# Kernel optimization log

Hardware: AMD Instinct MI355X
Metric: run time of the kernel (lower is better)

## Reference

```python
import jax, jax.numpy as jnp
import numpy as np

N, L, DS, DP, H, A, Q, V = 1, 512, 384, 256, 12, 16, 4, 8
SHID = H * (DP + A + 3 * V + V)  # 3648
WC = float(np.sqrt(2.0 / (9.0 * Q)))
WL = float(np.sqrt(1.0 / 3.0))
EPS = 1e-5


def quat2rot(q):
    # q: (..., 3) partial quaternion (w fixed to 1, then normalized) -> (..., 3, 3)
    ones = jnp.ones(q.shape[:-1] + (1,), q.dtype)
    qf = jnp.concatenate([ones, q], axis=-1)
    qf = qf / jnp.linalg.norm(qf, axis=-1, keepdims=True)
    w, x, y, z = qf[..., 0], qf[..., 1], qf[..., 2], qf[..., 3]
    r0 = jnp.stack([1 - 2 * (y * y + z * z), 2 * (x * y - w * z), 2 * (x * z + w * y)], -1)
    r1 = jnp.stack([2 * (x * y + w * z), 1 - 2 * (x * x + z * z), 2 * (y * z - w * x)], -1)
    r2 = jnp.stack([2 * (x * z - w * y), 2 * (y * z + w * x), 1 - 2 * (x * x + y * y)], -1)
    return jnp.stack([r0, r1, r2], axis=-2)


def layer_norm(x, g, b):
    m = x.mean(-1, keepdims=True)
    v = ((x - m) ** 2).mean(-1, keepdims=True)
    return (x - m) / jnp.sqrt(v + EPS) * g + b


def setup_inputs() -> dict:
    key = jax.random.key(0)
    ks = jax.random.split(key, 24)
    w = lambda k, shape, s=0.02: (jax.random.normal(k, shape, jnp.float32) * s)
    return {
        'sfea': jax.random.normal(ks[0], (N, L, DS), jnp.float32),
        'pfea': jax.random.normal(ks[1], (N, L, L, DP), jnp.float32),
        'quat': jax.random.normal(ks[2], (N, L, 3), jnp.float32) * 0.1,
        'trsl': jax.random.normal(ks[3], (N, L, 3), jnp.float32),
        'Wq': w(ks[4], (DS, H * A)), 'Wk': w(ks[5], (DS, H * A)), 'Wv': w(ks[6], (DS, H * A)),
        'Wqp': w(ks[7], (DS, H * Q * 3)), 'Wkp': w(ks[8], (DS, H * Q * 3)), 'Wvp': w(ks[9], (DS, H * V * 3)),
        'Wb': w(ks[10], (DP, H)),
        'scale': jnp.ones((H,), jnp.float32),
        'Ws': w(ks[11], (SHID, DS)), 'bs': jnp.zeros((DS,), jnp.float32),
        'W1': w(ks[12], (DS, DS)), 'b1': jnp.zeros((DS,), jnp.float32),
        'W2': w(ks[13], (DS, DS)), 'b2': jnp.zeros((DS,), jnp.float32),
        'W3': w(ks[14], (DS, DS)), 'b3': jnp.zeros((DS,), jnp.float32),
        'g1': jnp.ones((DS,), jnp.float32), 'be1': jnp.zeros((DS,), jnp.float32),
        'g2': jnp.ones((DS,), jnp.float32), 'be2': jnp.zeros((DS,), jnp.float32),
    }


def reference(sfea, pfea, quat, trsl, Wq, Wk, Wv, Wqp, Wkp, Wvp, Wb, scale, Ws, bs,
              W1, b1, W2, b2, W3, b3, g1, be1, g2, be2):
    n, l = sfea.shape[0], sfea.shape[1]
    # projections
    q = (sfea @ Wq).reshape(n, l, H, A)
    k = (sfea @ Wk).reshape(n, l, H, A)
    v = (sfea @ Wv).reshape(n, l, H, A)
    qp = (sfea @ Wqp).reshape(n, l, H, Q, 3)
    kp = (sfea @ Wkp).reshape(n, l, H, Q, 3)
    vp = (sfea @ Wvp).reshape(n, l, H, V, 3)
    b = jnp.einsum('nijp,ph->nijh', pfea, Wb)
    # local frames
    rot = quat2rot(quat)  # (n, l, 3, 3)
    t = trsl[:, :, None, None, :]
    qp_g = jnp.einsum('nlij,nlhqj->nlhqi', rot, qp) + t
    kp_g = jnp.einsum('nlij,nlhqj->nlhqi', rot, kp) + t
    vp_g = jnp.einsum('nlij,nlhvj->nlhvi', rot, vp) + t
    # attention logits
    qk = jnp.einsum('nihd,njhd->nijh', q, k) / np.sqrt(A)
    diff = qp_g[:, :, None] - kp_g[:, None]  # (n, i, j, h, q, 3)
    d2 = jnp.sum(diff * diff, axis=(-1, -2))  # (n, i, j, h)
    qkp = (WC * jax.nn.softplus(scale) / 2.0) * d2
    a = jax.nn.softmax(WL * (qk + b - qkp), axis=2)  # (n, i, j, h)
    # weighted sums (einsum avoids huge broadcast intermediates)
    op = jnp.einsum('nijh,nijp->nihp', a, pfea)
    ov = jnp.einsum('nijh,njhd->nihd', a, v)
    ovp_g = jnp.einsum('nijh,njhvc->nihvc', a, vp_g)
    # map back into local frame: R^T (x - t)
    ovp = jnp.einsum('nlji,nlhvj->nlhvi', rot, ovp_g - t)
    ovp_norm = jnp.sqrt(jnp.sum(ovp * ovp, axis=-1))  # (n, l, h, v)
    shid = jnp.concatenate([op, ov, ovp.reshape(n, l, H, V * 3), ovp_norm], axis=-1)
    shid = shid.reshape(n, l, SHID)
    # output projection + residual, post-LN, MLP, post-LN (v1 path, p_drop=0)
    s = sfea + shid @ Ws + bs
    s = layer_norm(s, g1, be1)
    h = jax.nn.relu(s @ W1 + b1)
    h = jax.nn.relu(h @ W2 + b2)
    s = s + (h @ W3 + b3)
    s = layer_norm(s, g2, be2)
    return s
```

## Files before the change

### kernel.cpp

```cpp
#include <hip/hip_runtime.h>
#include <cstddef>

typedef __attribute__((ext_vector_type(8))) short short8;
typedef __attribute__((ext_vector_type(4))) float f32x4;

#define WC_CONST 0.2357022603955158f
#define WL_CONST 0.5773502691896258f

__device__ __forceinline__ unsigned short rne_bf16(float f) {
  unsigned int u = __float_as_uint(f);
  u += 0x7fffu + ((u >> 16) & 1u);
  return (unsigned short)(u >> 16);
}

__global__ __launch_bounds__(256) void concat_w_kernel(
    const float* __restrict__ Wq, const float* __restrict__ Wk, const float* __restrict__ Wv,
    const float* __restrict__ Wqp, const float* __restrict__ Wkp, const float* __restrict__ Wvp,
    float* __restrict__ Wcat) {
  int idx = blockIdx.x * 256 + threadIdx.x;
  if (idx >= 384 * 1152) return;
  int k = idx / 1152, c = idx % 1152;
  float v;
  if (c < 192)       v = Wq [k*192 + c];
  else if (c < 384)  v = Wk [k*192 + (c-192)];
  else if (c < 576)  v = Wv [k*192 + (c-384)];
  else if (c < 720)  v = Wqp[k*144 + (c-576)];
  else if (c < 864)  v = Wkp[k*144 + (c-720)];
  else               v = Wvp[k*288 + (c-864)];
  Wcat[idx] = v;
}

__global__ __launch_bounds__(256) void gemm64_kernel(
    const float* __restrict__ Amat, const float* __restrict__ Bmat, float* __restrict__ Cp,
    int M, int N, int K, int ksl) {
  __shared__ float As[16][68];
  __shared__ float Bs[16][68];
  int t = threadIdx.x;
  int bn = blockIdx.x, bm = blockIdx.y, bz = blockIdx.z;
  int k0 = bz * ksl;
  int tr = t >> 4, tc = t & 15;
  int lm = t >> 2, lk4 = (t & 3) << 2;
  int lkb = t >> 4, lnq = (t & 15) << 2;
  const float* Ab = Amat + (size_t)(bm*64 + lm) * K;
  const float* Bb = Bmat + bn*64 + lnq;
  float acc[4][4];
  #pragma unroll
  for (int a2 = 0; a2 < 4; a2++)
    #pragma unroll
    for (int b2 = 0; b2 < 4; b2++) acc[a2][b2] = 0.f;

  for (int k = k0; k < k0 + ksl; k += 16) {
    float4 av = *(const float4*)(Ab + k + lk4);
    float4 bv = *(const float4*)(Bb + (size_t)(k + lkb) * N);
    As[lk4+0][lm] = av.x; As[lk4+1][lm] = av.y; As[lk4+2][lm] = av.z; As[lk4+3][lm] = av.w;
    *(float4*)&Bs[lkb][lnq] = bv;
    __syncthreads();
    #pragma unroll
    for (int kk = 0; kk < 16; kk++) {
      float4 a4 = *(const float4*)&As[kk][tr << 2];
      float4 b4 = *(const float4*)&Bs[kk][tc << 2];
      float ar[4] = {a4.x, a4.y, a4.z, a4.w};
      float br[4] = {b4.x, b4.y, b4.z, b4.w};
      #pragma unroll
      for (int a2 = 0; a2 < 4; a2++)
        #pragma unroll
        for (int b2 = 0; b2 < 4; b2++) acc[a2][b2] += ar[a2] * br[b2];
    }
    __syncthreads();
  }
  float* Cb = Cp + (size_t)bz * M * N + (size_t)(bm*64 + (tr << 2)) * N + bn*64 + (tc << 2);
  #pragma unroll
  for (int r = 0; r < 4; r++) {
    float4 o = {acc[r][0], acc[r][1], acc[r][2], acc[r][3]};
    *(float4*)(Cb + (size_t)r * N) = o;
  }
}

__global__ __launch_bounds__(256) void reduce_kernel(
    const float* __restrict__ Cp, float* __restrict__ out, const float* __restrict__ bias,
    int relu, int MN, int N, int sk) {
  int idx = blockIdx.x * 256 + threadIdx.x;
  if (idx >= MN) return;
  float s = 0.f;
  for (int z = 0; z < sk; z++) s += Cp[(size_t)z * MN + idx];
  if (bias) s += bias[idx % N];
  if (relu) s = fmaxf(s, 0.f);
  out[idx] = s;
}

__global__ __launch_bounds__(64) void frames_kernel(
    const float* __restrict__ proj, const float* __restrict__ quat, const float* __restrict__ trsl,
    float* __restrict__ rotb, float* __restrict__ qpg, float* __restrict__ kpg,
    float* __restrict__ vpg) {
  int i = blockIdx.x, t = threadIdx.x;
  float q0 = quat[i*3+0], q1 = quat[i*3+1], q2 = quat[i*3+2];
  float inv = rsqrtf(1.f + q0*q0 + q1*q1 + q2*q2);
  float w = inv, x = q0*inv, y = q1*inv, z = q2*inv;
  float R00 = 1.f - 2.f*(y*y + z*z), R01 = 2.f*(x*y - w*z), R02 = 2.f*(x*z + w*y);
  float R10 = 2.f*(x*y + w*z), R11 = 1.f - 2.f*(x*x + z*z), R12 = 2.f*(y*z - w*x);
  float R20 = 2.f*(x*z - w*y), R21 = 2.f*(y*z + w*x), R22 = 1.f - 2.f*(x*x + y*y);
  float t0 = trsl[i*3+0], t1 = trsl[i*3+1], t2 = trsl[i*3+2];
  if (t == 0) {
    float* rb = rotb + i*9;
    rb[0]=R00; rb[1]=R01; rb[2]=R02; rb[3]=R10; rb[4]=R11; rb[5]=R12; rb[6]=R20; rb[7]=R21; rb[8]=R22;
  }
  for (int pt = t; pt < 192; pt += 64) {
    const float* src; float* dst;
    if (pt < 48)      { src = proj + i*1152 + 576 + pt*3;        dst = qpg + i*144 + pt*3; }
    else if (pt < 96) { src = proj + i*1152 + 720 + (pt-48)*3;   dst = kpg + i*144 + (pt-48)*3; }
    else              { src = proj + i*1152 + 864 + (pt-96)*3;   dst = vpg + i*288 + (pt-96)*3; }
    float p0 = src[0], p1 = src[1], p2 = src[2];
    dst[0] = R00*p0 + R01*p1 + R02*p2 + t0;
    dst[1] = R10*p0 + R11*p1 + R12*p2 + t1;
    dst[2] = R20*p0 + R21*p1 + R22*p2 + t2;
  }
}

__device__ __forceinline__ float lt1_val(
    const float* __restrict__ proj, const float* __restrict__ kpg,
    const float* qs_, const float* qps_, float coef, int jg, int h) {
  const float4* kr = (const float4*)(proj + (size_t)jg*1152 + 192 + h*16);
  const float4* qr = (const float4*)(qs_ + h*16);
  float qk = 0.f;
  #pragma unroll
  for (int m = 0; m < 4; m++) {
    float4 kv = kr[m], qv = qr[m];
    qk += qv.x*kv.x + qv.y*kv.y + qv.z*kv.z + qv.w*kv.w;
  }
  const float4* kpr = (const float4*)(kpg + (size_t)jg*144 + h*12);
  const float4* qpr = (const float4*)(qps_ + h*12);
  float d2 = 0.f;
  #pragma unroll
  for (int m = 0; m < 3; m++) {
    float4 kv = kpr[m], qv = qpr[m];
    float dx = qv.x-kv.x, dy = qv.y-kv.y, dz = qv.z-kv.z, dw = qv.w-kv.w;
    d2 += dx*dx + dy*dy + dz*dz + dw*dw;
  }
  return qk*0.25f - coef*d2;
}

__global__ __launch_bounds__(768) void attn2_kernel(
    const float* __restrict__ proj, const float* __restrict__ qpg,
    const float* __restrict__ kpg, const float* __restrict__ vpg,
    const float* __restrict__ pfea, const float* __restrict__ Wb,
    const float* __restrict__ rotb, const float* __restrict__ trsl,
    const float* __restrict__ scale, float* __restrict__ shid) {
  __shared__ __align__(16) float P[32][260];
  __shared__ __align__(16) float Lw[512][12];
  __shared__ short wbf[8][64][8];
  __shared__ float Lb[2][32][12];
  __shared__ __align__(16) float qs[12][16];
  __shared__ __align__(16) float qps[12][12];
  __shared__ float coefs[12];
  __shared__ float sh_inv[12];
  __shared__ float rot_s[9];
  __shared__ float ovpg_l[12][24];

  int i = blockIdx.x;
  int t = threadIdx.x;
  int w = t >> 6, lane = t & 63;

  for (int idx = t; idx < 192; idx += 768) qs[idx >> 4][idx & 15] = proj[i*1152 + idx];
  for (int idx = t; idx < 144; idx += 768) qps[idx / 12][idx % 12] = qpg[i*144 + idx];
  if (t < 12) coefs[t] = WC_CONST * 0.5f * log1pf(__expf(scale[t]));
  if (t < 9)  rot_s[t] = rotb[i*9 + t];
  for (int s2 = t; s2 < 512; s2 += 768) {
    int ks = s2 >> 6, l = s2 & 63;
    int col = l & 15, kb = ks * 32 + ((l >> 4) << 3);
    #pragma unroll
    for (int j = 0; j < 8; j++)
      wbf[ks][l][j] = (col < 12) ? (short)rne_bf16(Wb[(kb + j) * 12 + col]) : (short)0;
  }
  __syncthreads();

  float4 opacc[12];
  #pragma unroll
  for (int h = 0; h < 12; h++) { opacc[h].x = 0.f; opacc[h].y = 0.f; opacc[h].z = 0.f; opacc[h].w = 0.f; }
  float4 streg[8];

  if (w >= 8) {
    int rbase = (w - 8) * 8;
    const float* src = pfea + (size_t)i * 131072;
    #pragma unroll
    for (int q2 = 0; q2 < 8; q2++)
      streg[q2] = *(const float4*)(src + (size_t)(rbase + q2) * 256 + (lane << 2));
  } else if (w >= 2) {
    int e = (w - 2) * 64 + lane;
    int jl = e / 12, h = e - jl * 12;
    Lb[0][jl][h] = lt1_val(proj, kpg, &qs[0][0], &qps[0][0], coefs[h], jl, h);
  }

  for (int tt = 0; tt < 16; tt++) {
    __syncthreads();
    if (w >= 8) {
      int rbase = (w - 8) * 8;
      #pragma unroll
      for (int q2 = 0; q2 < 8; q2++)
        *(float4*)&P[rbase + q2][lane << 2] = streg[q2];
    }
    __syncthreads();
    if (w < 2) {
      f32x4 accb = {0.f, 0.f, 0.f, 0.f};
      int row = (w << 4) + (lane & 15);
      int kq = lane >> 4;
      const float* Pb = &P[row][kq * 8];
      #pragma unroll
      for (int ks = 0; ks < 8; ks++) {
        float4 f0 = *(const float4*)(Pb + ks * 32);
        float4 f1 = *(const float4*)(Pb + ks * 32 + 4);
        short8 af;
        af[0] = (short)rne_bf16(f0.x); af[1] = (short)rne_bf16(f0.y);
        af[2] = (short)rne_bf16(f0.z); af[3] = (short)rne_bf16(f0.w);
        af[4] = (short)rne_bf16(f1.x); af[5] = (short)rne_bf16(f1.y);
        af[6] = (short)rne_bf16(f1.z); af[7] = (short)rne_bf16(f1.w);
        short8 bfv = *(const short8*)(&wbf[ks][lane][0]);
        accb = __builtin_amdgcn_mfma_f32_16x16x32_bf16(af, bfv, accb, 0, 0, 0);
      }
      int h = lane & 15;
      if (h < 12) {
        #pragma unroll
        for (int r = 0; r < 4; r++) {
          int jl = (w << 4) + kq * 4 + r;
          float lv = Lb[tt & 1][jl][h] + accb[r];
          Lw[tt * 32 + jl][h] = __expf(WL_CONST * lv);
        }
      }
    } else if (w < 8) {
      if (tt < 15) {
        int e = (w - 2) * 64 + lane;
        int jl = e / 12, h = e - jl * 12;
        Lb[(tt + 1) & 1][jl][h] =
            lt1_val(proj, kpg, &qs[0][0], &qps[0][0], coefs[h], (tt + 1) * 32 + jl, h);
      }
    } else {
      if (tt < 15) {
        int rbase = (w - 8) * 8;
        const float* src = pfea + (size_t)i * 131072 + (size_t)(tt + 1) * 32 * 256;
        #pragma unroll
        for (int q2 = 0; q2 < 8; q2++)
          streg[q2] = *(const float4*)(src + (size_t)(rbase + q2) * 256 + (lane << 2));
      }
    }
    __syncthreads();
    for (int rr = w; rr < 32; rr += 12) {
      const float4* lwp = (const float4*)&Lw[tt * 32 + rr][0];
      float4 wa = lwp[0], wb2 = lwp[1], wc = lwp[2];
      float4 pv = *(const float4*)&P[rr][lane << 2];
      opacc[0].x += pv.x*wa.x; opacc[0].y += pv.y*wa.x; opacc[0].z += pv.z*wa.x; opacc[0].w += pv.w*wa.x;
      opacc[1].x += pv.x*wa.y; opacc[1].y += pv.y*wa.y; opacc[1].z += pv.z*wa.y; opacc[1].w += pv.w*wa.y;
      opacc[2].x += pv.x*wa.z; opacc[2].y += pv.y*wa.z; opacc[2].z += pv.z*wa.z; opacc[2].w += pv.w*wa.z;
      opacc[3].x += pv.x*wa.w; opacc[3].y += pv.y*wa.w; opacc[3].z += pv.z*wa.w; opacc[3].w += pv.w*wa.w;
      opacc[4].x += pv.x*wb2.x; opacc[4].y += pv.y*wb2.x; opacc[4].z += pv.z*wb2.x; opacc[4].w += pv.w*wb2.x;
      opacc[5].x += pv.x*wb2.y; opacc[5].y += pv.y*wb2.y; opacc[5].z += pv.z*wb2.y; opacc[5].w += pv.w*wb2.y;
      opacc[6].x += pv.x*wb2.z; opacc[6].y += pv.y*wb2.z; opacc[6].z += pv.z*wb2.z; opacc[6].w += pv.w*wb2.z;
      opacc[7].x += pv.x*wb2.w; opacc[7].y += pv.y*wb2.w; opacc[7].z += pv.z*wb2.w; opacc[7].w += pv.w*wb2.w;
      opacc[8].x += pv.x*wc.x; opacc[8].y += pv.y*wc.x; opacc[8].z += pv.z*wc.x; opacc[8].w += pv.w*wc.x;
      opacc[9].x += pv.x*wc.y; opacc[9].y += pv.y*wc.y; opacc[9].z += pv.z*wc.y; opacc[9].w += pv.w*wc.y;
      opacc[10].x += pv.x*wc.z; opacc[10].y += pv.y*wc.z; opacc[10].z += pv.z*wc.z; opacc[10].w += pv.w*wc.z;
      opacc[11].x += pv.x*wc.w; opacc[11].y += pv.y*wc.w; opacc[11].z += pv.z*wc.w; opacc[11].w += pv.w*wc.w;
    }
  }
  __syncthreads();

  if (w < 12) {
    float sacc = 0.f;
    #pragma unroll
    for (int r2 = 0; r2 < 8; r2++) sacc += Lw[r2 * 64 + lane][w];
    #pragma unroll
    for (int off = 32; off >= 1; off >>= 1) sacc += __shfl_xor(sacc, off);
    if (lane == 0) sh_inv[w] = 1.0f / sacc;
  }
  __syncthreads();

  float4* Pred = (float4*)&P[0][0];
  #pragma unroll
  for (int gr = 0; gr < 6; gr++) {
    Pred[(w * 2 + 0) * 64 + lane] = opacc[2 * gr + 0];
    Pred[(w * 2 + 1) * 64 + lane] = opacc[2 * gr + 1];
    __syncthreads();
    if (t < 128) {
      int hh = t >> 6, ll = t & 63;
      float4 sum = {0.f, 0.f, 0.f, 0.f};
      #pragma unroll
      for (int w2 = 0; w2 < 12; w2++) {
        float4 v = Pred[(w2 * 2 + hh) * 64 + ll];
        sum.x += v.x; sum.y += v.y; sum.z += v.z; sum.w += v.w;
      }
      int h = 2 * gr + hh;
      float isv = sh_inv[h];
      float4 o = {sum.x * isv, sum.y * isv, sum.z * isv, sum.w * isv};
      *(float4*)(shid + (size_t)i * 3648 + h * 304 + (ll << 2)) = o;
    }
    __syncthreads();
  }

  if (t < 192) {
    int h = t >> 4, d = t & 15;
    const float* vb = proj + 384 + h * 16 + d;
    float acc = 0.f;
    #pragma unroll 8
    for (int j = 0; j < 512; j++) acc += Lw[j][h] * vb[(size_t)j * 1152];
    shid[(size_t)i * 3648 + h * 304 + 256 + d] = acc * sh_inv[h];
  } else if (t >= 256 && t < 544) {
    int idx = t - 256, h = idx / 24, m2 = idx % 24;
    const float* vb = vpg + h * 24 + m2;
    float acc = 0.f;
    #pragma unroll 8
    for (int j = 0; j < 512; j++) acc += Lw[j][h] * vb[(size_t)j * 288];
    ovpg_l[h][m2] = acc * sh_inv[h];
  }
  __syncthreads();

  if (t < 96) {
    int h = t >> 3, vv = t & 7;
    float x = ovpg_l[h][vv*3+0] - trsl[i*3+0];
    float y = ovpg_l[h][vv*3+1] - trsl[i*3+1];
    float z = ovpg_l[h][vv*3+2] - trsl[i*3+2];
    float o0 = rot_s[0]*x + rot_s[3]*y + rot_s[6]*z;
    float o1 = rot_s[1]*x + rot_s[4]*y + rot_s[7]*z;
    float o2 = rot_s[2]*x + rot_s[5]*y + rot_s[8]*z;
    float* so = shid + (size_t)i*3648 + h*304 + 272 + vv*3;
    so[0] = o0; so[1] = o1; so[2] = o2;
    shid[(size_t)i*3648 + h*304 + 296 + vv] = sqrtf(o0*o0 + o1*o1 + o2*o2);
  }
}

__global__ __launch_bounds__(384) void ln384_kernel(
    const float* __restrict__ resid, const float* __restrict__ C, const float* __restrict__ bias,
    const float* __restrict__ g, const float* __restrict__ be, float* __restrict__ out) {
  int i = blockIdx.x, t = threadIdx.x;
  __shared__ float red[6];
  float x = resid[(size_t)i*384 + t] + C[(size_t)i*384 + t] + bias[t];
  float s = x;
  #pragma unroll
  for (int off = 32; off >= 1; off >>= 1) s += __shfl_xor(s, off);
  if ((t & 63) == 0) red[t >> 6] = s;
  __syncthreads();
  float m = (red[0]+red[1]+red[2]+red[3]+red[4]+red[5]) * (1.f/384.f);
  __syncthreads();
  float d = x - m;
  float v = d * d;
  #pragma unroll
  for (int off = 32; off >= 1; off >>= 1) v += __shfl_xor(v, off);
  if ((t & 63) == 0) red[t >> 6] = v;
  __syncthreads();
  float var = (red[0]+red[1]+red[2]+red[3]+red[4]+red[5]) * (1.f/384.f);
  out[(size_t)i*384 + t] = d * rsqrtf(var + 1e-5f) * g[t] + be[t];
}

extern "C" void kernel_launch(void* const* d_in, const int* in_sizes, int n_in,
                              void* d_out, int out_size, void* d_ws, size_t ws_size,
                              hipStream_t stream) {
  const float* sfea = (const float*)d_in[0];
  const float* pfea = (const float*)d_in[1];
  const float* quat = (const float*)d_in[2];
  const float* trsl = (const float*)d_in[3];
  const float* Wq   = (const float*)d_in[4];
  const float* Wk   = (const float*)d_in[5];
  const float* Wv   = (const float*)d_in[6];
  const float* Wqp  = (const float*)d_in[7];
  const float* Wkp  = (const float*)d_in[8];
  const float* Wvp  = (const float*)d_in[9];
  const float* Wb   = (const float*)d_in[10];
  const float* scale= (const float*)d_in[11];
  const float* Wsm  = (const float*)d_in[12];
  const float* bs   = (const float*)d_in[13];
  const float* W1   = (const float*)d_in[14];
  const float* b1   = (const float*)d_in[15];
  const float* W2   = (const float*)d_in[16];
  const float* b2   = (const float*)d_in[17];
  const float* W3   = (const float*)d_in[18];
  const float* b3   = (const float*)d_in[19];
  const float* g1   = (const float*)d_in[20];
  const float* be1  = (const float*)d_in[21];
  const float* g2   = (const float*)d_in[22];
  const float* be2  = (const float*)d_in[23];
  float* out = (float*)d_out;
  float* wsf = (float*)d_ws;

  float* Wcat = wsf;
  float* proj = Wcat + 442368;
  float* rotb = proj + 589824;
  float* qpg  = rotb + 4608;
  float* kpg  = qpg + 73728;
  float* vpg  = kpg + 73728;
  float* shid = vpg + 147456;
  float* cpart= shid + 1867776;
  float* C1   = cpart + 1179648;
  float* s1   = C1 + 196608;
  float* h1   = s1 + 196608;
  float* h2   = h1 + 196608;
  float* C3   = h2 + 196608;

  concat_w_kernel<<<1728, 256, 0, stream>>>(Wq, Wk, Wv, Wqp, Wkp, Wvp, Wcat);
  gemm64_kernel<<<dim3(18, 8, 1), 256, 0, stream>>>(sfea, Wcat, proj, 512, 1152, 384, 384);
  frames_kernel<<<512, 64, 0, stream>>>(proj, quat, trsl, rotb, qpg, kpg, vpg);
  attn2_kernel<<<512, 768, 0, stream>>>(proj, qpg, kpg, vpg, pfea, Wb, rotb, trsl, scale, shid);

  gemm64_kernel<<<dim3(6, 8, 6), 256, 0, stream>>>(shid, Wsm, cpart, 512, 384, 3648, 608);
  reduce_kernel<<<768, 256, 0, stream>>>(cpart, C1, nullptr, 0, 196608, 384, 6);
  ln384_kernel<<<512, 384, 0, stream>>>(sfea, C1, bs, g1, be1, s1);

  gemm64_kernel<<<dim3(6, 8, 3), 256, 0, stream>>>(s1, W1, cpart, 512, 384, 384, 128);
  reduce_kernel<<<768, 256, 0, stream>>>(cpart, h1, b1, 1, 196608, 384, 3);
  gemm64_kernel<<<dim3(6, 8, 3), 256, 0, stream>>>(h1, W2, cpart, 512, 384, 384, 128);
  reduce_kernel<<<768, 256, 0, stream>>>(cpart, h2, b2, 1, 196608, 384, 3);
  gemm64_kernel<<<dim3(6, 8, 3), 256, 0, stream>>>(h2, W3, cpart, 512, 384, 384, 128);
  reduce_kernel<<<768, 256, 0, stream>>>(cpart, C3, nullptr, 0, 196608, 384, 3);
  ln384_kernel<<<512, 384, 0, stream>>>(s1, C3, b3, g2, be2, out);
}
```

Baseline: 308.0 us.

## Restructure attention with async LDS loads and fuse MLP GEMM epilogues

The attention kernel now streams the pair features in 16-row tiles straight into double-buffered shared memory with global_load_lds, instead of staging them through registers. Work is respecialised across warps: one wave does the bias MFMA, three compute logits, four issue loads, six accumulate the pair-feature sum, and the rest accumulate the value and point-value sums inside the main loop rather than in separate serial loops at the end. The MLP replaces split-K GEMMs plus reduce kernels with a single 32x32-tile GEMM that applies bias and ReLU in its epilogue, cutting launches and partial-sum traffic. The risks are more barriers from doubling the tile count, lower per-wave parallelism in the pair-feature reduction, and a small GEMM tile with little register reuse.

```diff
diff --git a/kernel.cpp b/kernel.cpp
--- a/kernel.cpp
+++ b/kernel.cpp
@@ -11,6 +11,13 @@
   unsigned int u = __float_as_uint(f);
   u += 0x7fffu + ((u >> 16) & 1u);
   return (unsigned short)(u >> 16);
+}
+
+typedef const __attribute__((address_space(1))) unsigned int* gas_u32;
+typedef __attribute__((address_space(3))) unsigned int* las_u32;
+
+__device__ __forceinline__ void gl_lds16(const float* g, float* l) {
+  __builtin_amdgcn_global_load_lds((gas_u32)(const void*)g, (las_u32)(void*)l, 16, 0, 0);
 }
 
 __global__ __launch_bounds__(256) void concat_w_kernel(
@@ -88,6 +95,43 @@
   out[idx] = s;
 }
 
+__global__ __launch_bounds__(256) void gemm32_kernel(
+    const float* __restrict__ Amat, const float* __restrict__ Bmat,
+    const float* __restrict__ bias,
+    float* __restrict__ C, int M, int N, int K, int relu) {
+  __shared__ float As[16][34];
+  __shared__ float Bs[16][34];
+  int t = threadIdx.x;
+  int bn = blockIdx.x, bm = blockIdx.y;
+  int tr = t >> 4, tc = t & 15;
+  int lm = t >> 3, lk2 = (t & 7) << 1;
+  int lkb = t >> 4, ln2 = (t & 15) << 1;
+  const float* Ab = Amat + (size_t)(bm*32 + lm) * K;
+  const float* Bb = Bmat + bn*32 + ln2;
+  float a00=0.f, a01=0.f, a10=0.f, a11=0.f;
+  for (int k = 0; k < K; k += 16) {
+    float2 av = *(const float2*)(Ab + k + lk2);
+    float2 bv = *(const float2*)(Bb + (size_t)(k + lkb) * N);
+    As[lk2][lm] = av.x; As[lk2+1][lm] = av.y;
+    *(float2*)&Bs[lkb][ln2] = bv;
+    __syncthreads();
+    #pragma unroll
+    for (int kk = 0; kk < 16; kk++) {
+      float2 a2 = *(const float2*)&As[kk][tr << 1];
+      float2 b2 = *(const float2*)&Bs[kk][tc << 1];
+      a00 += a2.x*b2.x; a01 += a2.x*b2.y; a10 += a2.y*b2.x; a11 += a2.y*b2.y;
+    }
+    __syncthreads();
+  }
+  int r0 = bm*32 + (tr << 1), c0 = bn*32 + (tc << 1);
+  float bb0 = bias ? bias[c0] : 0.f, bb1 = bias ? bias[c0+1] : 0.f;
+  float o00 = a00 + bb0, o01 = a01 + bb1, o10 = a10 + bb0, o11 = a11 + bb1;
+  if (relu) { o00=fmaxf(o00,0.f); o01=fmaxf(o01,0.f); o10=fmaxf(o10,0.f); o11=fmaxf(o11,0.f); }
+  float2 w0 = {o00, o01}, w1 = {o10, o11};
+  *(float2*)(C + (size_t)r0*N + c0) = w0;
+  *(float2*)(C + (size_t)(r0+1)*N + c0) = w1;
+}
+
 __global__ __launch_bounds__(64) void frames_kernel(
     const float* __restrict__ proj, const float* __restrict__ quat, const float* __restrict__ trsl,
     float* __restrict__ rotb, float* __restrict__ qpg, float* __restrict__ kpg,
@@ -139,25 +183,23 @@
   return qk*0.25f - coef*d2;
 }
 
-__global__ __launch_bounds__(768) void attn2_kernel(
+__global__ __launch_bounds__(768, 6) void attn3_kernel(
     const float* __restrict__ proj, const float* __restrict__ qpg,
     const float* __restrict__ kpg, const float* __restrict__ vpg,
     const float* __restrict__ pfea, const float* __restrict__ Wb,
     const float* __restrict__ rotb, const float* __restrict__ trsl,
     const float* __restrict__ scale, float* __restrict__ shid) {
-  __shared__ __align__(16) float P[32][260];
+  __shared__ __align__(16) float P[2][16][260];
   __shared__ __align__(16) float Lw[512][12];
   __shared__ short wbf[8][64][8];
-  __shared__ float Lb[2][32][12];
+  __shared__ float Lb[2][16][12];
   __shared__ __align__(16) float qs[12][16];
   __shared__ __align__(16) float qps[12][12];
-  __shared__ float coefs[12];
-  __shared__ float sh_inv[12];
-  __shared__ float rot_s[9];
+  __shared__ float coefs[12], sh_inv[12], rot_s[9];
+  __shared__ __align__(16) float redbuf[2048];
   __shared__ float ovpg_l[12][24];
 
-  int i = blockIdx.x;
-  int t = threadIdx.x;
+  int i = blockIdx.x, t = threadIdx.x;
   int w = t >> 6, lane = t & 63;
 
   for (int idx = t; idx < 192; idx += 768) qs[idx >> 4][idx & 15] = proj[i*1152 + idx];
@@ -173,37 +215,33 @@
   }
   __syncthreads();
 
-  float4 opacc[12];
-  #pragma unroll
-  for (int h = 0; h < 12; h++) { opacc[h].x = 0.f; opacc[h].y = 0.f; opacc[h].z = 0.f; opacc[h].w = 0.f; }
-  float4 streg[8];
-
-  if (w >= 8) {
-    int rbase = (w - 8) * 8;
-    const float* src = pfea + (size_t)i * 131072;
-    #pragma unroll
-    for (int q2 = 0; q2 < 8; q2++)
-      streg[q2] = *(const float4*)(src + (size_t)(rbase + q2) * 256 + (lane << 2));
-  } else if (w >= 2) {
-    int e = (w - 2) * 64 + lane;
+  if (w >= 1 && w <= 3) {
+    int e = (w - 1) * 64 + lane;
     int jl = e / 12, h = e - jl * 12;
     Lb[0][jl][h] = lt1_val(proj, kpg, &qs[0][0], &qps[0][0], coefs[h], jl, h);
-  }
-
-  for (int tt = 0; tt < 16; tt++) {
-    __syncthreads();
-    if (w >= 8) {
-      int rbase = (w - 8) * 8;
-      #pragma unroll
-      for (int q2 = 0; q2 < 8; q2++)
-        *(float4*)&P[rbase + q2][lane << 2] = streg[q2];
-    }
-    __syncthreads();
-    if (w < 2) {
+  } else if (w >= 4 && w <= 7) {
+    int r = (w - 4) * 4;
+    const float* src = pfea + (size_t)i * 131072 + lane * 4;
+    #pragma unroll
+    for (int q = 0; q < 4; q++) gl_lds16(src + (size_t)(r + q) * 256, &P[0][r + q][0]);
+  }
+  __syncthreads();
+
+  float4 acc4[4];
+  #pragma unroll
+  for (int c = 0; c < 4; c++) { acc4[c].x=0.f; acc4[c].y=0.f; acc4[c].z=0.f; acc4[c].w=0.f; }
+  float accv[3] = {0.f, 0.f, 0.f};
+  float accvp[5] = {0.f, 0.f, 0.f, 0.f, 0.f};
+  int hv0 = lane >> 4, hv1 = 4 + (lane >> 4), hv2 = 8 + (lane >> 4);
+  int hp0 = lane / 24, hp1 = (lane + 64) / 24, hp2 = (lane + 128) / 24,
+      hp3 = (lane + 192) / 24, hp4 = (lane + 256) / 24;
+
+  int cur = 0;
+  for (int tt = 0; tt < 32; tt++) {
+    if (w == 0) {
       f32x4 accb = {0.f, 0.f, 0.f, 0.f};
-      int row = (w << 4) + (lane & 15);
-      int kq = lane >> 4;
-      const float* Pb = &P[row][kq * 8];
+      int row = lane & 15, kq = lane >> 4;
+      const float* Pb = &P[cur][row][kq * 8];
       #pragma unroll
       for (int ks = 0; ks < 8; ks++) {
         float4 f0 = *(const float4*)(Pb + ks * 32);
@@ -220,94 +258,117 @@
       if (h < 12) {
         #pragma unroll
         for (int r = 0; r < 4; r++) {
-          int jl = (w << 4) + kq * 4 + r;
-          float lv = Lb[tt & 1][jl][h] + accb[r];
-          Lw[tt * 32 + jl][h] = __expf(WL_CONST * lv);
+          int jl = kq * 4 + r;
+          Lw[tt * 16 + jl][h] = __expf(WL_CONST * (Lb[tt & 1][jl][h] + accb[r]));
         }
       }
-    } else if (w < 8) {
-      if (tt < 15) {
-        int e = (w - 2) * 64 + lane;
+    } else if (w <= 3) {
+      if (tt < 31) {
+        int e = (w - 1) * 64 + lane;
         int jl = e / 12, h = e - jl * 12;
         Lb[(tt + 1) & 1][jl][h] =
-            lt1_val(proj, kpg, &qs[0][0], &qps[0][0], coefs[h], (tt + 1) * 32 + jl, h);
+            lt1_val(proj, kpg, &qs[0][0], &qps[0][0], coefs[h], (tt + 1) * 16 + jl, h);
+      }
+    } else if (w <= 7) {
+      if (tt < 31) {
+        int r = (w - 4) * 4;
+        const float* src = pfea + (size_t)i * 131072 + (size_t)(tt + 1) * 4096 + lane * 4;
+        #pragma unroll
+        for (int q = 0; q < 4; q++) gl_lds16(src + (size_t)(r + q) * 256, &P[cur ^ 1][r + q][0]);
+      }
+    }
+    asm volatile("s_waitcnt lgkmcnt(0)" ::: "memory");
+    __builtin_amdgcn_sched_barrier(0);
+    __builtin_amdgcn_s_barrier();
+    __builtin_amdgcn_sched_barrier(0);
+    if (w < 6) {
+      int qd = w >> 1, rp = w & 1;
+      #pragma unroll
+      for (int r = 0; r < 16; r += 2) {
+        int rr = r + rp;
+        float4 lq = *(const float4*)&Lw[tt * 16 + rr][qd * 4];
+        float4 pv = *(const float4*)&P[cur][rr][lane << 2];
+        acc4[0].x += pv.x*lq.x; acc4[0].y += pv.y*lq.x; acc4[0].z += pv.z*lq.x; acc4[0].w += pv.w*lq.x;
+        acc4[1].x += pv.x*lq.y; acc4[1].y += pv.y*lq.y; acc4[1].z += pv.z*lq.y; acc4[1].w += pv.w*lq.y;
+        acc4[2].x += pv.x*lq.z; acc4[2].y += pv.y*lq.z; acc4[2].z += pv.z*lq.z; acc4[2].w += pv.w*lq.z;
+        acc4[3].x += pv.x*lq.w; acc4[3].y += pv.y*lq.w; acc4[3].z += pv.z*lq.w; acc4[3].w += pv.w*lq.w;
+      }
+    } else if (w < 10) {
+      #pragma unroll
+      for (int q = 0; q < 4; q++) {
+        int j = tt * 16 + (w - 6) * 4 + q;
+        const float* vrow = proj + (size_t)j * 1152 + 384;
+        accv[0] += Lw[j][hv0] * vrow[lane];
+        accv[1] += Lw[j][hv1] * vrow[64 + lane];
+        accv[2] += Lw[j][hv2] * vrow[128 + lane];
       }
     } else {
-      if (tt < 15) {
-        int rbase = (w - 8) * 8;
-        const float* src = pfea + (size_t)i * 131072 + (size_t)(tt + 1) * 32 * 256;
-        #pragma unroll
-        for (int q2 = 0; q2 < 8; q2++)
-          streg[q2] = *(const float4*)(src + (size_t)(rbase + q2) * 256 + (lane << 2));
-      }
-    }
-    __syncthreads();
-    for (int rr = w; rr < 32; rr += 12) {
-      const float4* lwp = (const float4*)&Lw[tt * 32 + rr][0];
-      float4 wa = lwp[0], wb2 = lwp[1], wc = lwp[2];
-      float4 pv = *(const float4*)&P[rr][lane << 2];
-      opacc[0].x += pv.x*wa.x; opacc[0].y += pv.y*wa.x; opacc[0].z += pv.z*wa.x; opacc[0].w += pv.w*wa.x;
-      opacc[1].x += pv.x*wa.y; opacc[1].y += pv.y*wa.y; opacc[1].z += pv.z*wa.y; opacc[1].w += pv.w*wa.y;
-      opacc[2].x += pv.x*wa.z; opacc[2].y += pv.y*wa.z; opacc[2].z += pv.z*wa.z; opacc[2].w += pv.w*wa.z;
-      opacc[3].x += pv.x*wa.w; opacc[3].y += pv.y*wa.w; opacc[3].z += pv.z*wa.w; opacc[3].w += pv.w*wa.w;
-      opacc[4].x += pv.x*wb2.x; opacc[4].y += pv.y*wb2.x; opacc[4].z += pv.z*wb2.x; opacc[4].w += pv.w*wb2.x;
-      opacc[5].x += pv.x*wb2.y; opacc[5].y += pv.y*wb2.y; opacc[5].z += pv.z*wb2.y; opacc[5].w += pv.w*wb2.y;
-      opacc[6].x += pv.x*wb2.z; opacc[6].y += pv.y*wb2.z; opacc[6].z += pv.z*wb2.z; opacc[6].w += pv.w*wb2.z;
-      opacc[7].x += pv.x*wb2.w; opacc[7].y += pv.y*wb2.w; opacc[7].z += pv.z*wb2.w; opacc[7].w += pv.w*wb2.w;
-      opacc[8].x += pv.x*wc.x; opacc[8].y += pv.y*wc.x; opacc[8].z += pv.z*wc.x; opacc[8].w += pv.w*wc.x;
-      opacc[9].x += pv.x*wc.y; opacc[9].y += pv.y*wc.y; opacc[9].z += pv.z*wc.y; opacc[9].w += pv.w*wc.y;
-      opacc[10].x += pv.x*wc.z; opacc[10].y += pv.y*wc.z; opacc[10].z += pv.z*wc.z; opacc[10].w += pv.w*wc.z;
-      opacc[11].x += pv.x*wc.w; opacc[11].y += pv.y*wc.w; opacc[11].z += pv.z*wc.w; opacc[11].w += pv.w*wc.w;
-    }
-  }
-  __syncthreads();
-
-  if (w < 12) {
+      #pragma unroll
+      for (int q = 0; q < 8; q++) {
+        int j = tt * 16 + (w - 10) * 8 + q;
+        const float* vprow = vpg + (size_t)j * 288;
+        accvp[0] += Lw[j][hp0] * vprow[lane];
+        accvp[1] += Lw[j][hp1] * vprow[64 + lane];
+        accvp[2] += Lw[j][hp2] * vprow[128 + lane];
+        accvp[3] += Lw[j][hp3] * vprow[192 + lane];
+        if (lane < 32) accvp[4] += Lw[j][hp4] * vprow[256 + lane];
+      }
+    }
+    __syncthreads();
+    cur ^= 1;
+  }
+
+  {
     float sacc = 0.f;
     #pragma unroll
-    for (int r2 = 0; r2 < 8; r2++) sacc += Lw[r2 * 64 + lane][w];
+    for (int r2 = 0; r2 < 8; r2++) sacc += Lw[lane + 64 * r2][w];
     #pragma unroll
     for (int off = 32; off >= 1; off >>= 1) sacc += __shfl_xor(sacc, off);
-    if (lane == 0) sh_inv[w] = 1.0f / sacc;
-  }
-  __syncthreads();
-
-  float4* Pred = (float4*)&P[0][0];
-  #pragma unroll
-  for (int gr = 0; gr < 6; gr++) {
-    Pred[(w * 2 + 0) * 64 + lane] = opacc[2 * gr + 0];
-    Pred[(w * 2 + 1) * 64 + lane] = opacc[2 * gr + 1];
-    __syncthreads();
-    if (t < 128) {
-      int hh = t >> 6, ll = t & 63;
-      float4 sum = {0.f, 0.f, 0.f, 0.f};
-      #pragma unroll
-      for (int w2 = 0; w2 < 12; w2++) {
-        float4 v = Pred[(w2 * 2 + hh) * 64 + ll];
-        sum.x += v.x; sum.y += v.y; sum.z += v.z; sum.w += v.w;
-      }
-      int h = 2 * gr + hh;
+    if (lane == 0 && w < 12) sh_inv[w] = 1.0f / sacc;
+  }
+  __syncthreads();
+
+  float4* rb4 = (float4*)redbuf;
+  #pragma unroll
+  for (int qd2 = 0; qd2 < 3; qd2++) {
+    if (w < 6 && (w >> 1) == qd2) {
+      int half = w & 1;
+      #pragma unroll
+      for (int c = 0; c < 4; c++) rb4[half * 256 + c * 64 + lane] = acc4[c];
+    }
+    __syncthreads();
+    if (t < 256) {
+      int c = t >> 6, ll = t & 63;
+      float4 s0 = rb4[c * 64 + ll], s1 = rb4[256 + c * 64 + ll];
+      int h = qd2 * 4 + c;
       float isv = sh_inv[h];
-      float4 o = {sum.x * isv, sum.y * isv, sum.z * isv, sum.w * isv};
+      float4 o = {(s0.x + s1.x) * isv, (s0.y + s1.y) * isv,
+                  (s0.z + s1.z) * isv, (s0.w + s1.w) * isv};
       *(float4*)(shid + (size_t)i * 3648 + h * 304 + (ll << 2)) = o;
     }
     __syncthreads();
   }
 
+  if (w >= 6 && w < 10) {
+    int sl = w - 6;
+    redbuf[sl * 192 + lane]       = accv[0];
+    redbuf[sl * 192 + 64 + lane]  = accv[1];
+    redbuf[sl * 192 + 128 + lane] = accv[2];
+  } else if (w >= 10) {
+    int sl = w - 10;
+    #pragma unroll
+    for (int k = 0; k < 4; k++) redbuf[768 + sl * 288 + lane + 64 * k] = accvp[k];
+    if (lane < 32) redbuf[768 + sl * 288 + 256 + lane] = accvp[4];
+  }
+  __syncthreads();
   if (t < 192) {
-    int h = t >> 4, d = t & 15;
-    const float* vb = proj + 384 + h * 16 + d;
-    float acc = 0.f;
-    #pragma unroll 8
-    for (int j = 0; j < 512; j++) acc += Lw[j][h] * vb[(size_t)j * 1152];
-    shid[(size_t)i * 3648 + h * 304 + 256 + d] = acc * sh_inv[h];
+    int h = t >> 4;
+    float s = (redbuf[t] + redbuf[192 + t] + redbuf[384 + t] + redbuf[576 + t]) * sh_inv[h];
+    shid[(size_t)i * 3648 + h * 304 + 256 + (t & 15)] = s;
   } else if (t >= 256 && t < 544) {
-    int idx = t - 256, h = idx / 24, m2 = idx % 24;
-    const float* vb = vpg + h * 24 + m2;
-    float acc = 0.f;
-    #pragma unroll 8
-    for (int j = 0; j < 512; j++) acc += Lw[j][h] * vb[(size_t)j * 288];
-    ovpg_l[h][m2] = acc * sh_inv[h];
+    int m = t - 256, h = m / 24;
+    float s = (redbuf[768 + m] + redbuf[768 + 288 + m]) * sh_inv[h];
+    ovpg_l[h][m - h * 24] = s;
   }
   __syncthreads();
 
@@ -395,17 +456,14 @@
   concat_w_kernel<<<1728, 256, 0, stream>>>(Wq, Wk, Wv, Wqp, Wkp, Wvp, Wcat);
   gemm64_kernel<<<dim3(18, 8, 1), 256, 0, stream>>>(sfea, Wcat, proj, 512, 1152, 384, 384);
   frames_kernel<<<512, 64, 0, stream>>>(proj, quat, trsl, rotb, qpg, kpg, vpg);
-  attn2_kernel<<<512, 768, 0, stream>>>(proj, qpg, kpg, vpg, pfea, Wb, rotb, trsl, scale, shid);
+  attn3_kernel<<<512, 768, 0, stream>>>(proj, qpg, kpg, vpg, pfea, Wb, rotb, trsl, scale, shid);
 
   gemm64_kernel<<<dim3(6, 8, 6), 256, 0, stream>>>(shid, Wsm, cpart, 512, 384, 3648, 608);
   reduce_kernel<<<768, 256, 0, stream>>>(cpart, C1, nullptr, 0, 196608, 384, 6);
   ln384_kernel<<<512, 384, 0, stream>>>(sfea, C1, bs, g1, be1, s1);
 
-  gemm64_kernel<<<dim3(6, 8, 3), 256, 0, stream>>>(s1, W1, cpart, 512, 384, 384, 128);
-  reduce_kernel<<<768, 256, 0, stream>>>(cpart, h1, b1, 1, 196608, 384, 3);
-  gemm64_kernel<<<dim3(6, 8, 3), 256, 0, stream>>>(h1, W2, cpart, 512, 384, 384, 128);
-  reduce_kernel<<<768, 256, 0, stream>>>(cpart, h2, b2, 1, 196608, 384, 3);
-  gemm64_kernel<<<dim3(6, 8, 3), 256, 0, stream>>>(h2, W3, cpart, 512, 384, 384, 128);
-  reduce_kernel<<<768, 256, 0, stream>>>(cpart, C3, nullptr, 0, 196608, 384, 3);
+  gemm32_kernel<<<dim3(12, 16), 256, 0, stream>>>(s1, W1, b1, h1, 512, 384, 384, 1);
+  gemm32_kernel<<<dim3(12, 16), 256, 0, stream>>>(h1, W2, b2, h2, 512, 384, 384, 1);
+  gemm32_kernel<<<dim3(12, 16), 256, 0, stream>>>(h2, W3, nullptr, C3, 512, 384, 384, 0);
   ln384_kernel<<<512, 384, 0, stream>>>(s1, C3, b3, g2, be2, out);
 }
```

Result: slower. 585.3 us (+90.0%).
